# Optimization experiments

Measured on AMD Instinct MI355X. Metric: run time of the kernel, lower is better.

Reference implementation:

```python
import jax, jax.numpy as jnp
import numpy as np
import math

B, T, N, D = 2, 2048, 16, 128


def setup_inputs() -> dict:
    key = jax.random.key(0)
    ks = jax.random.split(key, 9)
    s = 1.0 / math.sqrt(D)
    return {
        "x": jax.random.normal(ks[0], (B, T, N, D), dtype=jnp.float32),
        "wq": jax.random.normal(ks[1], (D, D), dtype=jnp.float32) * s,
        "bq": jax.random.normal(ks[2], (D,), dtype=jnp.float32) * 0.02,
        "wk": jax.random.normal(ks[3], (D, D), dtype=jnp.float32) * s,
        "bk": jax.random.normal(ks[4], (D,), dtype=jnp.float32) * 0.02,
        "wv": jax.random.normal(ks[5], (D, D), dtype=jnp.float32) * s,
        "bv": jax.random.normal(ks[6], (D,), dtype=jnp.float32) * 0.02,
        "wp": jax.random.normal(ks[7], (D, D), dtype=jnp.float32) * s,
        "bp": jax.random.normal(ks[8], (D,), dtype=jnp.float32) * 0.02,
    }


def reference(x, wq, bq, wk, bk, wv, bv, wp, bp):
    # x: (B, T, N, D); per-head Linear projections (torch y = x @ W.T + b)
    d = x.shape[-1]
    q = jnp.einsum("btnd,ed->btne", x, wq) + bq  # (B,T,N,D)
    k = jnp.einsum("btnd,ed->btne", x, wk) + bk
    v = jnp.einsum("btnd,ed->btne", x, wv) + bv
    scale = 1.0 / jnp.sqrt(jnp.asarray(d, dtype=x.dtype))
    # scores: (B, N, T, T)
    scores = jnp.einsum("btnd,bsnd->bnts", q, k) * scale
    t = scores.shape[-1]
    causal = jnp.tril(jnp.ones((t, t), dtype=bool))  # (T,T)
    scores = jnp.where(causal[None, None], scores, jnp.asarray(-jnp.inf, scores.dtype))
    w = jax.nn.softmax(scores, axis=-1)
    att = jnp.einsum("bnts,bsnd->btnd", w, v)  # (B,T,N,D)
    out = jnp.einsum("btnd,ed->btne", att, wp) + bp
    return out
```

## Files before the change

kernel.cpp:

```cpp
#include <hip/hip_runtime.h>
#include <cmath>

#define BB 2
#define TT 2048
#define NN 16
#define DD 128
#define NROWS (BB*TT*NN)
#define PLANE (TT*DD)
#define KP 132
#define VP 68

typedef unsigned short u16;
typedef unsigned int   u32;
typedef __attribute__((ext_vector_type(8)))  short s8v;
typedef __attribute__((ext_vector_type(16))) float vf16;

__device__ u16 g_Q [(size_t)NROWS * DD];
__device__ u16 g_K [(size_t)NROWS * DD];
__device__ u16 g_V [(size_t)NROWS * DD];
__device__ u16 g_VT[(size_t)NROWS * DD];

__device__ __forceinline__ u16 f2bf(float f) {
    return (u16)((__float_as_uint(f) + 0x8000u) >> 16);
}
__device__ __forceinline__ u32 pk2(float a, float b) {
    return ((__float_as_uint(a) + 0x8000u) >> 16)
         | ((__float_as_uint(b) + 0x8000u) & 0xFFFF0000u);
}
__device__ __forceinline__ void st8(u16* p, const float4& a, const float4& b) {
    uint2 lo, hi;
    lo.x = pk2(a.x, a.y); lo.y = pk2(a.z, a.w);
    hi.x = pk2(b.x, b.y); hi.y = pk2(b.z, b.w);
    *(uint2*)p       = lo;
    *(uint2*)(p + 4) = hi;
}
__device__ __forceinline__ s8v ld8(const u16* p) {
    short4 a = *(const short4*)p;
    short4 b = *(const short4*)(p + 4);
    return (s8v){a.x, a.y, a.z, a.w, b.x, b.y, b.z, b.w};
}

__global__ __launch_bounds__(256)
void qkv_proj_kernel(const float* __restrict__ x,
                     const float* __restrict__ Wq, const float* __restrict__ Bq,
                     const float* __restrict__ Wk, const float* __restrict__ Bk,
                     const float* __restrict__ Wv, const float* __restrict__ Bv)
{
    __shared__ u16 Xs[128*KP];
    __shared__ u16 Ws[128*KP];

    const int t  = threadIdx.x;
    const int r0 = blockIdx.x * 128;
    const float4* xsrc = (const float4*)(x + (size_t)r0*DD);

    #pragma unroll
    for (int it = 0; it < 8; ++it) {
        int i = t + 256*it;
        int e = i >> 4, c8 = i & 15;
        st8(&Xs[e*KP + c8*8], xsrc[2*i], xsrc[2*i + 1]);
    }
    #pragma unroll
    for (int it = 0; it < 8; ++it) {
        int i = t + 256*it;
        int e = i >> 4, c8 = i & 15;
        st8(&Ws[e*KP + c8*8], ((const float4*)Wq)[2*i], ((const float4*)Wq)[2*i + 1]);
    }
    __syncthreads();

    const int w   = t >> 6;
    const int l31 = t & 31;
    const int q2  = (t >> 5) & 1;

    s8v af[8];
    #pragma unroll
    for (int s = 0; s < 8; ++s)
        af[s] = ld8(&Xs[(w*32 + l31)*KP + s*16 + q2*8]);

    #pragma unroll
    for (int wsel = 0; wsel < 3; ++wsel) {
        const float* Bi = (wsel == 0) ? Bq : (wsel == 1) ? Bk : Bv;
        u16*         Ot = (wsel == 0) ? g_Q : (wsel == 1) ? g_K : g_V;

        vf16 acc[4];
        #pragma unroll
        for (int et = 0; et < 4; ++et)
            #pragma unroll
            for (int i = 0; i < 16; ++i) acc[et][i] = 0.f;

        #pragma unroll
        for (int s = 0; s < 8; ++s) {
            #pragma unroll
            for (int et = 0; et < 4; ++et) {
                s8v bf = ld8(&Ws[(et*32 + l31)*KP + s*16 + q2*8]);
                acc[et] = __builtin_amdgcn_mfma_f32_32x32x16_bf16(af[s], bf, acc[et], 0, 0, 0);
            }
        }

        float bb[4];
        #pragma unroll
        for (int et = 0; et < 4; ++et) bb[et] = Bi[et*32 + l31];

        #pragma unroll
        for (int r = 0; r < 16; ++r) {
            int rl = (r & 3) + 8*(r >> 2) + 4*q2;
            int rg = r0 + w*32 + rl;
            int b = rg >> 15, rem = rg & 32767;
            int tt = rem >> 4, n = rem & 15;
            size_t orow = (size_t)((b*NN + n)*TT + tt) * DD;
            #pragma unroll
            for (int et = 0; et < 4; ++et) {
                float ov = acc[et][r] + bb[et];
                if (wsel == 0) ov *= 0.12752053685940512f;
                Ot[orow + et*32 + l31] = f2bf(ov);
            }
        }

        if (wsel < 2) {
            const float* Wn = (wsel == 0) ? Wk : Wv;
            __syncthreads();
            #pragma unroll
            for (int it = 0; it < 8; ++it) {
                int i = t + 256*it;
                int e = i >> 4, c8 = i & 15;
                st8(&Ws[e*KP + c8*8], ((const float4*)Wn)[2*i], ((const float4*)Wn)[2*i + 1]);
            }
            __syncthreads();
        }
    }
}

__global__ __launch_bounds__(256)
void out_proj_kernel(const float* __restrict__ W, const float* __restrict__ Bi,
                     float* __restrict__ out)
{
    __shared__ u16 Ws[128*KP];

    const int t  = threadIdx.x;
    const int r0 = blockIdx.x * 128;

    #pragma unroll
    for (int it = 0; it < 8; ++it) {
        int i = t + 256*it;
        int e = i >> 4, c8 = i & 15;
        st8(&Ws[e*KP + c8*8], ((const float4*)W)[2*i], ((const float4*)W)[2*i + 1]);
    }

    const int w   = t >> 6;
    const int l31 = t & 31;
    const int q2  = (t >> 5) & 1;

    s8v af[8];
    {
        const u16* src = g_Q + (size_t)(r0 + w*32 + l31)*DD;
        #pragma unroll
        for (int s = 0; s < 8; ++s)
            af[s] = *(const s8v*)&src[s*16 + q2*8];
    }
    __syncthreads();

    vf16 acc[4];
    #pragma unroll
    for (int et = 0; et < 4; ++et)
        #pragma unroll
        for (int i = 0; i < 16; ++i) acc[et][i] = 0.f;

    #pragma unroll
    for (int s = 0; s < 8; ++s) {
        #pragma unroll
        for (int et = 0; et < 4; ++et) {
            s8v bf = ld8(&Ws[(et*32 + l31)*KP + s*16 + q2*8]);
            acc[et] = __builtin_amdgcn_mfma_f32_32x32x16_bf16(af[s], bf, acc[et], 0, 0, 0);
        }
    }

    float bb[4];
    #pragma unroll
    for (int et = 0; et < 4; ++et) bb[et] = Bi[et*32 + l31];

    #pragma unroll
    for (int r = 0; r < 16; ++r) {
        int rl = (r & 3) + 8*(r >> 2) + 4*q2;
        int rg = r0 + w*32 + rl;
        int b = rg >> 15, rem = rg & 32767;
        int n = rem >> 11, tt = rem & 2047;
        size_t orow = (size_t)((b*TT + tt)*NN + n) * DD;
        #pragma unroll
        for (int et = 0; et < 4; ++et)
            out[orow + et*32 + l31] = acc[et][r] + bb[et];
    }
}

__global__ __launch_bounds__(256)
void vtrans_kernel()
{
    __shared__ u16 L[64*KP];

    const int t   = threadIdx.x;
    const int blk = blockIdx.x;
    const int pl  = blk >> 5;
    const int tt0 = (blk & 31) * 64;
    const size_t plane = (size_t)pl * PLANE;

    #pragma unroll
    for (int c = 0; c < 4; ++c) {
        int j = t + 256*c;
        int row = j >> 4, c16 = j & 15;
        uint4 v = *(const uint4*)&g_V[plane + (size_t)(tt0 + row)*DD + c16*8];
        *(uint4*)&L[row*KP + c16*8] = v;
    }
    __syncthreads();
    #pragma unroll
    for (int c = 0; c < 4; ++c) {
        int j = t + 256*c;
        int d = j >> 3, tc = j & 7;
        u16 e[8];
        #pragma unroll
        for (int i = 0; i < 8; ++i) e[i] = L[(tc*8 + i)*KP + d];
        uint4 pkv;
        pkv.x = (u32)e[0] | ((u32)e[1] << 16);
        pkv.y = (u32)e[2] | ((u32)e[3] << 16);
        pkv.z = (u32)e[4] | ((u32)e[5] << 16);
        pkv.w = (u32)e[6] | ((u32)e[7] << 16);
        *(uint4*)&g_VT[plane + (size_t)d*TT + tt0 + tc*8] = pkv;
    }
}

__global__ __launch_bounds__(128, 2)
void attn_kernel()
{
    __shared__ u16 Ks[64*KP];
    __shared__ u16 Vt[128*VP];

    const int t   = threadIdx.x;
    const int grp = blockIdx.x >> 5;
    const int bn  = blockIdx.x & 31;
    int qt;
    if      (grp < 8)  qt = 31 - grp;
    else if (grp < 16) qt = grp - 8;
    else if (grp < 24) qt = 39 - grp;
    else               qt = grp - 16;

    const size_t plane = (size_t)bn * PLANE;
    const u16* Kg = g_K  + plane;
    const u16* Vg = g_VT + plane;

    const int w      = t >> 6;
    const int lane   = t & 63;
    const int lane31 = lane & 31;
    const int q2     = lane >> 5;
    const int qband  = qt*64 + 32*w;
    const int qrow   = qband + lane31;

    s8v qf[8];
    {
        const u16* Qg = g_Q + plane + (size_t)qrow * DD;
        #pragma unroll
        for (int s = 0; s < 8; ++s)
            qf[s] = *(const s8v*)&Qg[s*16 + q2*8];
    }

    vf16 accO[4];
    #pragma unroll
    for (int dt = 0; dt < 4; ++dt)
        #pragma unroll
        for (int i = 0; i < 16; ++i) accO[dt][i] = 0.f;

    float mrow = -INFINITY, lrow = 0.f;

    const int nkt = qt + 1;

    uint4 pk[8], pv[8];
    #pragma unroll
    for (int c = 0; c < 8; ++c) {
        int j = t + 128*c;
        int kr = j >> 4, kc = j & 15;
        pk[c] = *(const uint4*)&Kg[kr*DD + kc*8];
        int vr = j >> 3, vc = j & 7;
        pv[c] = *(const uint4*)&Vg[(size_t)vr*TT + vc*8];
    }

    for (int kt = 0; kt < nkt; ++kt) {
        const int k0 = kt*64;
        __syncthreads();
        #pragma unroll
        for (int c = 0; c < 8; ++c) {
            int j = t + 128*c;
            int kr = j >> 4, kc = j & 15;
            uint2 a, b;
            a.x = pk[c].x; a.y = pk[c].y; b.x = pk[c].z; b.y = pk[c].w;
            *(uint2*)&Ks[kr*KP + kc*8]     = a;
            *(uint2*)&Ks[kr*KP + kc*8 + 4] = b;
            int vr = j >> 3, vc = j & 7;
            a.x = pv[c].x; a.y = pv[c].y; b.x = pv[c].z; b.y = pv[c].w;
            *(uint2*)&Vt[vr*VP + vc*8]     = a;
            *(uint2*)&Vt[vr*VP + vc*8 + 4] = b;
        }
        __syncthreads();

        if (kt + 1 < nkt) {
            const u16* Kg2 = Kg + (size_t)(k0 + 64)*DD;
            const u16* Vg2 = Vg + (k0 + 64);
            #pragma unroll
            for (int c = 0; c < 8; ++c) {
                int j = t + 128*c;
                int kr = j >> 4, kc = j & 15;
                pk[c] = *(const uint4*)&Kg2[kr*DD + kc*8];
                int vr = j >> 3, vc = j & 7;
                pv[c] = *(const uint4*)&Vg2[(size_t)vr*TT + vc*8];
            }
        }

        vf16 accS[2];
        #pragma unroll
        for (int kk = 0; kk < 2; ++kk)
            #pragma unroll
            for (int i = 0; i < 16; ++i) accS[kk][i] = 0.f;
        __builtin_amdgcn_s_setprio(1);
        #pragma unroll
        for (int s = 0; s < 8; ++s) {
            #pragma unroll
            for (int kk = 0; kk < 2; ++kk) {
                s8v a = ld8(&Ks[(kk*32 + lane31)*KP + s*16 + q2*8]);
                accS[kk] = __builtin_amdgcn_mfma_f32_32x32x16_bf16(a, qf[s], accS[kk], 0, 0, 0);
            }
        }
        __builtin_amdgcn_s_setprio(0);

        float p[2][16];
        const bool tail = (kt == qt);
        #pragma unroll
        for (int kk = 0; kk < 2; ++kk)
            #pragma unroll
            for (int r = 0; r < 16; ++r) {
                float sv = accS[kk][r];
                if (tail) {
                    int keyg = k0 + kk*32 + (r & 3) + 8*(r >> 2) + 4*q2;
                    if (keyg > qrow) sv = -INFINITY;
                }
                p[kk][r] = sv;
            }

        float v0 = -INFINITY, v1 = -INFINITY;
        #pragma unroll
        for (int r = 0; r < 16; ++r) {
            v0 = fmaxf(v0, p[0][r]);
            v1 = fmaxf(v1, p[1][r]);
        }
        float vmax = fmaxf(v0, v1);
        vmax = fmaxf(vmax, __shfl_xor(vmax, 32));

        if (!__all(vmax <= mrow + 8.f)) {
            float mnew  = fmaxf(mrow, vmax);
            float alpha = __builtin_amdgcn_exp2f(mrow - mnew);
            lrow *= alpha;
            float ar[16];
            #pragma unroll
            for (int r = 0; r < 16; ++r)
                ar[r] = __shfl(alpha, (r & 3) + 8*(r >> 2) + 4*q2);
            #pragma unroll
            for (int dt = 0; dt < 4; ++dt)
                #pragma unroll
                for (int r = 0; r < 16; ++r) accO[dt][r] *= ar[r];
            mrow = mnew;
        }

        float ls0 = 0.f, ls1 = 0.f;
        #pragma unroll
        for (int r = 0; r < 16; ++r) {
            float e0 = __builtin_amdgcn_exp2f(p[0][r] - mrow);
            float e1 = __builtin_amdgcn_exp2f(p[1][r] - mrow);
            p[0][r] = e0; p[1][r] = e1;
            ls0 += e0; ls1 += e1;
        }
        float ls = ls0 + ls1;
        ls += __shfl_xor(ls, 32);
        lrow += ls;

        s8v pf[4];
        #pragma unroll
        for (int tau = 0; tau < 4; ++tau) {
            int kk = tau >> 1, rb = (tau & 1)*8;
            s8v v;
            #pragma unroll
            for (int j = 0; j < 8; ++j)
                v[j] = (short)(__float_as_uint(p[kk][rb + j]) >> 16);
            pf[tau] = v;
        }

        __builtin_amdgcn_s_setprio(1);
        #pragma unroll
        for (int dt = 0; dt < 4; ++dt) {
            const u16* vp = &Vt[(dt*32 + lane31)*VP];
            #pragma unroll
            for (int tau = 0; tau < 4; ++tau) {
                const u16* q = vp + 16*tau + 4*q2;
                short4 lo = *(const short4*)q;
                short4 hi = *(const short4*)(q + 8);
                s8v bvv = {lo.x, lo.y, lo.z, lo.w, hi.x, hi.y, hi.z, hi.w};
                accO[dt] = __builtin_amdgcn_mfma_f32_32x32x16_bf16(pf[tau], bvv, accO[dt], 0, 0, 0);
            }
        }
        __builtin_amdgcn_s_setprio(0);
    }

    float inv = 1.0f / lrow;
    #pragma unroll
    for (int r = 0; r < 16; ++r) {
        int rl = (r & 3) + 8*(r >> 2) + 4*q2;
        float ir = __shfl(inv, rl);
        u16* op = g_Q + plane + (size_t)(qband + rl)*DD;
        #pragma unroll
        for (int dt = 0; dt < 4; ++dt)
            op[dt*32 + lane31] = f2bf(accO[dt][r] * ir);
    }
}

extern "C" void kernel_launch(void* const* d_in, const int* in_sizes, int n_in,
                              void* d_out, int out_size, void* d_ws, size_t ws_size,
                              hipStream_t stream)
{
    const float* x  = (const float*)d_in[0];
    const float* wq = (const float*)d_in[1];
    const float* bq = (const float*)d_in[2];
    const float* wk = (const float*)d_in[3];
    const float* bk = (const float*)d_in[4];
    const float* wv = (const float*)d_in[5];
    const float* bv = (const float*)d_in[6];
    const float* wp = (const float*)d_in[7];
    const float* bp = (const float*)d_in[8];
    float* out = (float*)d_out;
    (void)d_ws; (void)ws_size;

    qkv_proj_kernel<<<dim3(NROWS/128), dim3(256), 0, stream>>>(
        x, wq, bq, wk, bk, wv, bv);
    vtrans_kernel<<<dim3(BB*NN*(TT/64)), dim3(256), 0, stream>>>();
    attn_kernel<<<dim3(BB*NN*(TT/64)), dim3(128), 0, stream>>>();
    out_proj_kernel<<<dim3(NROWS/128), dim3(256), 0, stream>>>(wp, bp, out);
}
```

Measured before the change: 198.9 us.

## Double-buffer K/V tiles in LDS and enlarge attention query tile to 128 rows

Result: no change. 196.2 us (-1.3%).

```diff
diff --git a/kernel.cpp b/kernel.cpp
--- a/kernel.cpp
+++ b/kernel.cpp
@@ -225,21 +225,17 @@
     }
 }
 
-__global__ __launch_bounds__(128, 2)
+__global__ __launch_bounds__(256, 2)
 void attn_kernel()
 {
-    __shared__ u16 Ks[64*KP];
-    __shared__ u16 Vt[128*VP];
+    __shared__ u16 Ks[2][64*KP];
+    __shared__ u16 Vt[2][128*VP];
 
     const int t   = threadIdx.x;
     const int grp = blockIdx.x >> 5;
     const int bn  = blockIdx.x & 31;
-    int qt;
-    if      (grp < 8)  qt = 31 - grp;
-    else if (grp < 16) qt = grp - 8;
-    else if (grp < 24) qt = 39 - grp;
-    else               qt = grp - 16;
-
+    const int qt  = (grp < 8) ? (15 - grp) : (grp - 8);
+    const int q0  = qt * 128;
     const size_t plane = (size_t)bn * PLANE;
     const u16* Kg = g_K  + plane;
     const u16* Vg = g_VT + plane;
@@ -248,7 +244,7 @@
     const int lane   = t & 63;
     const int lane31 = lane & 31;
     const int q2     = lane >> 5;
-    const int qband  = qt*64 + 32*w;
+    const int qband  = q0 + 32*w;
     const int qrow   = qband + lane31;
 
     s8v qf[8];
@@ -266,141 +262,173 @@
         for (int i = 0; i < 16; ++i) accO[dt][i] = 0.f;
 
     float mrow = -INFINITY, lrow = 0.f;
-
-    const int nkt = qt + 1;
-
-    uint4 pk[8], pv[8];
-    #pragma unroll
-    for (int c = 0; c < 8; ++c) {
-        int j = t + 128*c;
+    const int nkt = 2*qt + 2;
+
+    uint4 pk[4], pv[4];
+
+    #pragma unroll
+    for (int c = 0; c < 4; ++c) {
+        int j = t + 256*c;
         int kr = j >> 4, kc = j & 15;
         pk[c] = *(const uint4*)&Kg[kr*DD + kc*8];
         int vr = j >> 3, vc = j & 7;
         pv[c] = *(const uint4*)&Vg[(size_t)vr*TT + vc*8];
     }
+    #pragma unroll
+    for (int c = 0; c < 4; ++c) {
+        int j = t + 256*c;
+        int kr = j >> 4, kc = j & 15;
+        uint2 a, b;
+        a.x = pk[c].x; a.y = pk[c].y; b.x = pk[c].z; b.y = pk[c].w;
+        *(uint2*)&Ks[0][kr*KP + kc*8]     = a;
+        *(uint2*)&Ks[0][kr*KP + kc*8 + 4] = b;
+        int vr = j >> 3, vc = j & 7;
+        a.x = pv[c].x; a.y = pv[c].y; b.x = pv[c].z; b.y = pv[c].w;
+        *(uint2*)&Vt[0][vr*VP + vc*8]     = a;
+        *(uint2*)&Vt[0][vr*VP + vc*8 + 4] = b;
+    }
+    {
+        const u16* Kg2 = Kg + (size_t)64*DD;
+        const u16* Vg2 = Vg + 64;
+        #pragma unroll
+        for (int c = 0; c < 4; ++c) {
+            int j = t + 256*c;
+            int kr = j >> 4, kc = j & 15;
+            pk[c] = *(const uint4*)&Kg2[kr*DD + kc*8];
+            int vr = j >> 3, vc = j & 7;
+            pv[c] = *(const uint4*)&Vg2[(size_t)vr*TT + vc*8];
+        }
+    }
 
     for (int kt = 0; kt < nkt; ++kt) {
         const int k0 = kt*64;
         __syncthreads();
-        #pragma unroll
-        for (int c = 0; c < 8; ++c) {
-            int j = t + 128*c;
-            int kr = j >> 4, kc = j & 15;
-            uint2 a, b;
-            a.x = pk[c].x; a.y = pk[c].y; b.x = pk[c].z; b.y = pk[c].w;
-            *(uint2*)&Ks[kr*KP + kc*8]     = a;
-            *(uint2*)&Ks[kr*KP + kc*8 + 4] = b;
-            int vr = j >> 3, vc = j & 7;
-            a.x = pv[c].x; a.y = pv[c].y; b.x = pv[c].z; b.y = pv[c].w;
-            *(uint2*)&Vt[vr*VP + vc*8]     = a;
-            *(uint2*)&Vt[vr*VP + vc*8 + 4] = b;
-        }
-        __syncthreads();
+        const u16* Kb = Ks[kt & 1];
+        const u16* Vb = Vt[kt & 1];
+
+        if (k0 <= qband + 31) {
+            vf16 accS[2];
+            #pragma unroll
+            for (int kk = 0; kk < 2; ++kk)
+                #pragma unroll
+                for (int i = 0; i < 16; ++i) accS[kk][i] = 0.f;
+            __builtin_amdgcn_s_setprio(1);
+            #pragma unroll
+            for (int s = 0; s < 8; ++s) {
+                #pragma unroll
+                for (int kk = 0; kk < 2; ++kk) {
+                    s8v a = ld8(&Kb[(kk*32 + lane31)*KP + s*16 + q2*8]);
+                    accS[kk] = __builtin_amdgcn_mfma_f32_32x32x16_bf16(a, qf[s], accS[kk], 0, 0, 0);
+                }
+            }
+            __builtin_amdgcn_s_setprio(0);
+
+            float p[2][16];
+            const bool tail = (k0 + 63 > qband);
+            #pragma unroll
+            for (int kk = 0; kk < 2; ++kk)
+                #pragma unroll
+                for (int r = 0; r < 16; ++r) {
+                    float sv = accS[kk][r];
+                    if (tail) {
+                        int keyg = k0 + kk*32 + (r & 3) + 8*(r >> 2) + 4*q2;
+                        if (keyg > qrow) sv = -INFINITY;
+                    }
+                    p[kk][r] = sv;
+                }
+
+            float v0 = -INFINITY, v1 = -INFINITY;
+            #pragma unroll
+            for (int r = 0; r < 16; ++r) {
+                v0 = fmaxf(v0, p[0][r]);
+                v1 = fmaxf(v1, p[1][r]);
+            }
+            float vmax = fmaxf(v0, v1);
+            vmax = fmaxf(vmax, __shfl_xor(vmax, 32));
+
+            if (!__all(vmax <= mrow + 8.f)) {
+                float mnew  = fmaxf(mrow, vmax);
+                float alpha = __builtin_amdgcn_exp2f(mrow - mnew);
+                lrow *= alpha;
+                float ar[16];
+                #pragma unroll
+                for (int r = 0; r < 16; ++r)
+                    ar[r] = __shfl(alpha, (r & 3) + 8*(r >> 2) + 4*q2);
+                #pragma unroll
+                for (int dt = 0; dt < 4; ++dt)
+                    #pragma unroll
+                    for (int r = 0; r < 16; ++r) accO[dt][r] *= ar[r];
+                mrow = mnew;
+            }
+
+            float ls0 = 0.f, ls1 = 0.f;
+            #pragma unroll
+            for (int r = 0; r < 16; ++r) {
+                float e0 = __builtin_amdgcn_exp2f(p[0][r] - mrow);
+                float e1 = __builtin_amdgcn_exp2f(p[1][r] - mrow);
+                p[0][r] = e0; p[1][r] = e1;
+                ls0 += e0; ls1 += e1;
+            }
+            float ls = ls0 + ls1;
+            ls += __shfl_xor(ls, 32);
+            lrow += ls;
+
+            s8v pf[4];
+            #pragma unroll
+            for (int tau = 0; tau < 4; ++tau) {
+                int kk = tau >> 1, rb = (tau & 1)*8;
+                s8v v;
+                #pragma unroll
+                for (int j = 0; j < 8; ++j)
+                    v[j] = (short)(__float_as_uint(p[kk][rb + j]) >> 16);
+                pf[tau] = v;
+            }
+
+            __builtin_amdgcn_s_setprio(1);
+            #pragma unroll
+            for (int dt = 0; dt < 4; ++dt) {
+                const u16* vp = &Vb[(dt*32 + lane31)*VP];
+                #pragma unroll
+                for (int tau = 0; tau < 4; ++tau) {
+                    const u16* q = vp + 16*tau + 4*q2;
+                    short4 lo = *(const short4*)q;
+                    short4 hi = *(const short4*)(q + 8);
+                    s8v bvv = {lo.x, lo.y, lo.z, lo.w, hi.x, hi.y, hi.z, hi.w};
+                    accO[dt] = __builtin_amdgcn_mfma_f32_32x32x16_bf16(pf[tau], bvv, accO[dt], 0, 0, 0);
+                }
+            }
+            __builtin_amdgcn_s_setprio(0);
+        }
 
         if (kt + 1 < nkt) {
-            const u16* Kg2 = Kg + (size_t)(k0 + 64)*DD;
-            const u16* Vg2 = Vg + (k0 + 64);
-            #pragma unroll
-            for (int c = 0; c < 8; ++c) {
-                int j = t + 128*c;
+            u16* Kw = Ks[(kt + 1) & 1];
+            u16* Vw = Vt[(kt + 1) & 1];
+            #pragma unroll
+            for (int c = 0; c < 4; ++c) {
+                int j = t + 256*c;
                 int kr = j >> 4, kc = j & 15;
-                pk[c] = *(const uint4*)&Kg2[kr*DD + kc*8];
+                uint2 a, b;
+                a.x = pk[c].x; a.y = pk[c].y; b.x = pk[c].z; b.y = pk[c].w;
+                *(uint2*)&Kw[kr*KP + kc*8]     = a;
+                *(uint2*)&Kw[kr*KP + kc*8 + 4] = b;
                 int vr = j >> 3, vc = j & 7;
-                pv[c] = *(const uint4*)&Vg2[(size_t)vr*TT + vc*8];
-            }
-        }
-
-        vf16 accS[2];
-        #pragma unroll
-        for (int kk = 0; kk < 2; ++kk)
-            #pragma unroll
-            for (int i = 0; i < 16; ++i) accS[kk][i] = 0.f;
-        __builtin_amdgcn_s_setprio(1);
-        #pragma unroll
-        for (int s = 0; s < 8; ++s) {
-            #pragma unroll
-            for (int kk = 0; kk < 2; ++kk) {
-                s8v a = ld8(&Ks[(kk*32 + lane31)*KP + s*16 + q2*8]);
-                accS[kk] = __builtin_amdgcn_mfma_f32_32x32x16_bf16(a, qf[s], accS[kk], 0, 0, 0);
-            }
-        }
-        __builtin_amdgcn_s_setprio(0);
-
-        float p[2][16];
-        const bool tail = (kt == qt);
-        #pragma unroll
-        for (int kk = 0; kk < 2; ++kk)
-            #pragma unroll
-            for (int r = 0; r < 16; ++r) {
-                float sv = accS[kk][r];
-                if (tail) {
-                    int keyg = k0 + kk*32 + (r & 3) + 8*(r >> 2) + 4*q2;
-                    if (keyg > qrow) sv = -INFINITY;
+                a.x = pv[c].x; a.y = pv[c].y; b.x = pv[c].z; b.y = pv[c].w;
+                *(uint2*)&Vw[vr*VP + vc*8]     = a;
+                *(uint2*)&Vw[vr*VP + vc*8 + 4] = b;
+            }
+            if (kt + 2 < nkt) {
+                const u16* Kg2 = Kg + (size_t)(k0 + 128)*DD;
+                const u16* Vg2 = Vg + (k0 + 128);
+                #pragma unroll
+                for (int c = 0; c < 4; ++c) {
+                    int j = t + 256*c;
+                    int kr = j >> 4, kc = j & 15;
+                    pk[c] = *(const uint4*)&Kg2[kr*DD + kc*8];
+                    int vr = j >> 3, vc = j & 7;
+                    pv[c] = *(const uint4*)&Vg2[(size_t)vr*TT + vc*8];
                 }
-                p[kk][r] = sv;
-            }
-
-        float v0 = -INFINITY, v1 = -INFINITY;
-        #pragma unroll
-        for (int r = 0; r < 16; ++r) {
-            v0 = fmaxf(v0, p[0][r]);
-            v1 = fmaxf(v1, p[1][r]);
-        }
-        float vmax = fmaxf(v0, v1);
-        vmax = fmaxf(vmax, __shfl_xor(vmax, 32));
-
-        if (!__all(vmax <= mrow + 8.f)) {
-            float mnew  = fmaxf(mrow, vmax);
-            float alpha = __builtin_amdgcn_exp2f(mrow - mnew);
-            lrow *= alpha;
-            float ar[16];
-            #pragma unroll
-            for (int r = 0; r < 16; ++r)
-                ar[r] = __shfl(alpha, (r & 3) + 8*(r >> 2) + 4*q2);
-            #pragma unroll
-            for (int dt = 0; dt < 4; ++dt)
-                #pragma unroll
-                for (int r = 0; r < 16; ++r) accO[dt][r] *= ar[r];
-            mrow = mnew;
-        }
-
-        float ls0 = 0.f, ls1 = 0.f;
-        #pragma unroll
-        for (int r = 0; r < 16; ++r) {
-            float e0 = __builtin_amdgcn_exp2f(p[0][r] - mrow);
-            float e1 = __builtin_amdgcn_exp2f(p[1][r] - mrow);
-            p[0][r] = e0; p[1][r] = e1;
-            ls0 += e0; ls1 += e1;
-        }
-        float ls = ls0 + ls1;
-        ls += __shfl_xor(ls, 32);
-        lrow += ls;
-
-        s8v pf[4];
-        #pragma unroll
-        for (int tau = 0; tau < 4; ++tau) {
-            int kk = tau >> 1, rb = (tau & 1)*8;
-            s8v v;
-            #pragma unroll
-            for (int j = 0; j < 8; ++j)
-                v[j] = (short)(__float_as_uint(p[kk][rb + j]) >> 16);
-            pf[tau] = v;
-        }
-
-        __builtin_amdgcn_s_setprio(1);
-        #pragma unroll
-        for (int dt = 0; dt < 4; ++dt) {
-            const u16* vp = &Vt[(dt*32 + lane31)*VP];
-            #pragma unroll
-            for (int tau = 0; tau < 4; ++tau) {
-                const u16* q = vp + 16*tau + 4*q2;
-                short4 lo = *(const short4*)q;
-                short4 hi = *(const short4*)(q + 8);
-                s8v bvv = {lo.x, lo.y, lo.z, lo.w, hi.x, hi.y, hi.z, hi.w};
-                accO[dt] = __builtin_amdgcn_mfma_f32_32x32x16_bf16(pf[tau], bvv, accO[dt], 0, 0, 0);
-            }
-        }
-        __builtin_amdgcn_s_setprio(0);
+            }
+        }
     }
 
     float inv = 1.0f / lrow;
@@ -434,6 +462,6 @@
     qkv_proj_kernel<<<dim3(NROWS/128), dim3(256), 0, stream>>>(
         x, wq, bq, wk, bk, wv, bv);
     vtrans_kernel<<<dim3(BB*NN*(TT/64)), dim3(256), 0, stream>>>();
-    attn_kernel<<<dim3(BB*NN*(TT/64)), dim3(128), 0, stream>>>();
+    attn_kernel<<<dim3(BB*NN*(TT/128)), dim3(256), 0, stream>>>();
     out_proj_kernel<<<dim3(NROWS/128), dim3(256), 0, stream>>>(wp, bp, out);
 }
```
